# Performance work log

Hardware: AMD Instinct MI355X
Metric: run time of the kernel (lower is better)

The kernel has to match this reference:

```python
import jax, jax.numpy as jnp
import numpy as np

N, P, D = 128, 256, 256
H, M = 16, 32            # num_heads, head_dim; output_dim = H*M = 512
OUT, HID = H * M, 2048


def setup_inputs() -> dict:
    key = jax.random.key(0)
    ks = jax.random.split(key, 7)
    s = 0.02
    return {
        "x": jax.random.normal(ks[0], (N, P, D), jnp.float32),
        "qkv_temporal": jax.random.normal(ks[1], (3, D, H, M), jnp.float32) * s,
        "qkv_point": jax.random.normal(ks[2], (3, H, M, H, M), jnp.float32) * s,
        "W1": jax.random.normal(ks[3], (OUT, HID), jnp.float32) * s,
        "b1": jnp.zeros((HID,), jnp.float32),
        "W2": jax.random.normal(ks[4], (HID, OUT), jnp.float32) * s,
        "b2": jnp.zeros((OUT,), jnp.float32),
    }


def reference(x, qkv_temporal, qkv_point, W1, b1, W2, b2):
    # ---- temporal attention (over frames i/I, per point j) ----
    qkv = jnp.einsum('wdhm,ijd->whmij', qkv_temporal, x)     # (3,H,M,N,P)
    q, k, v = qkv[0], qkv[1], qkv[2]
    scores = jnp.einsum('hmij,hmIj->hiIj', q, k)             # (H,N,N,P)
    weights = jax.nn.softmax(scores, axis=2)
    # NOTE: label order 'hIij' (positional) matches the original source exactly
    temporal = jnp.einsum('hIij,hmIj->hmij', weights, v)     # (H,M,N,P)
    # ---- point attention (over points j/J, per frame i) ----
    qkv = jnp.einsum('whmHM,HMij->whmij', qkv_point, temporal)  # (3,H,M,N,P)
    q, k, v = qkv[0], qkv[1], qkv[2]
    scores = jnp.einsum('hmij,hmiJ->hijJ', q, k)             # (H,N,P,P)
    weights = jax.nn.softmax(scores, axis=-1)
    pa = jnp.einsum('hijJ,hmiJ->ijhm', weights, v)           # (N,P,H,M)
    pa = pa.reshape(pa.shape[0], pa.shape[1], -1)            # (N,P,H*M)
    # ---- two-layer MLP (no activation, matching the source) ----
    h = pa @ W1 + b1
    return h @ W2 + b2
```

## Files before the change

### kernel.cpp

```cpp
#include <hip/hip_runtime.h>
#include <cstddef>
#include <cstdint>

constexpr int Nf = 128, Pp = 256, Dd = 256, Hh = 16, Mm = 32;
constexpr int OUTC = 512, HID = 2048, C3 = 1536;

typedef short short8 __attribute__((ext_vector_type(8)));
typedef float f32x4 __attribute__((ext_vector_type(4)));

__device__ inline unsigned short f2bf(float f) {
  unsigned u = __float_as_uint(f);
  u += 0x7fffu + ((u >> 16) & 1u);
  return (unsigned short)(u >> 16);
}
__device__ inline unsigned pk2(float a, float b) {
  return (unsigned)f2bf(a) | ((unsigned)f2bf(b) << 16);
}

__global__ __launch_bounds__(256) void conv_x(const float* __restrict__ x,
                                              short* __restrict__ xb) {
  int idx = blockIdx.x * 256 + threadIdx.x;
  const float4* s = (const float4*)x + (size_t)idx * 2;
  float4 a = s[0], c = s[1];
  uint4 o;
  o.x = pk2(a.x, a.y); o.y = pk2(a.z, a.w);
  o.z = pk2(c.x, c.y); o.w = pk2(c.z, c.w);
  ((uint4*)xb)[idx] = o;
}

__global__ __launch_bounds__(256) void transpose_to_bf16(const float* __restrict__ in,
                                                         short* __restrict__ out,
                                                         int R, int C) {
  __shared__ float tile[64 * 65];
  const int t = threadIdx.x;
  const int rb = blockIdx.y * 64, cb = blockIdx.x * 64;
  const size_t sl = (size_t)blockIdx.z * R * C;
#pragma unroll
  for (int u = 0; u < 4; ++u) {
    int r = (t >> 4) + u * 16, c4 = (t & 15) * 4;
    float4 v = *(const float4*)(in + sl + (size_t)(rb + r) * C + cb + c4);
    tile[r * 65 + c4 + 0] = v.x;
    tile[r * 65 + c4 + 1] = v.y;
    tile[r * 65 + c4 + 2] = v.z;
    tile[r * 65 + c4 + 3] = v.w;
  }
  __syncthreads();
#pragma unroll
  for (int u = 0; u < 2; ++u) {
    int id = t + u * 256;
    int n = id >> 3, kg = id & 7;
    float a[8];
#pragma unroll
    for (int q = 0; q < 8; ++q) a[q] = tile[(kg * 8 + q) * 65 + n];
    uint4 o;
    o.x = pk2(a[0], a[1]); o.y = pk2(a[2], a[3]);
    o.z = pk2(a[4], a[5]); o.w = pk2(a[6], a[7]);
    *(uint4*)(out + sl + (size_t)(cb + n) * R + rb + kg * 8) = o;
  }
}

__global__ void repack_b2t(const float* __restrict__ Wp, short* __restrict__ B2t) {
  int idx = blockIdx.x * 256 + threadIdx.x;
  int c = idx >> 9, k = idx & 511;
  int w = c >> 9, h = (c >> 5) & 15, m = c & 31;
  int HH = k >> 5, MM = k & 31;
  B2t[idx] = (short)f2bf(Wp[(((w * Hh + h) * Mm + m) * Hh + HH) * Mm + MM]);
}

__global__ __launch_bounds__(256) void wc_splitk(const short* __restrict__ A,
                                                 const short* __restrict__ Bt,
                                                 float* __restrict__ part) {
  __shared__ short As[128 * 32];
  __shared__ short Bs[128 * 32];
  const int t = threadIdx.x;
  const int wv = t >> 6, ln = t & 63;
  const int wr = wv >> 1, wc = wv & 1;
  const int lr = ln & 15, kq = ln >> 4;
  const int row0 = blockIdx.y * 128, col0 = blockIdx.x * 128;
  const int k0 = blockIdx.z * 256;

  f32x4 acc[4][4];
#pragma unroll
  for (int i = 0; i < 4; ++i)
#pragma unroll
    for (int j = 0; j < 4; ++j) acc[i][j] = {0.f, 0.f, 0.f, 0.f};

  for (int kt = k0; kt < k0 + 256; kt += 32) {
#pragma unroll
    for (int u = 0; u < 2; ++u) {
      int seg = wv * 128 + u * 64 + ln;
      int r = seg >> 2, kg = seg & 3;
      const short* gp = A + (size_t)(row0 + r) * HID + kt + kg * 8;
      __builtin_amdgcn_global_load_lds(
          (const __attribute__((address_space(1))) void*)gp,
          (__attribute__((address_space(3))) void*)&As[(wv * 128 + u * 64) * 8], 16, 0, 0);
    }
#pragma unroll
    for (int u = 0; u < 2; ++u) {
      int seg = wv * 128 + u * 64 + ln;
      int r = seg >> 2, kg = seg & 3;
      const short* gp = Bt + (size_t)(col0 + r) * HID + kt + kg * 8;
      __builtin_amdgcn_global_load_lds(
          (const __attribute__((address_space(1))) void*)gp,
          (__attribute__((address_space(3))) void*)&Bs[(wv * 128 + u * 64) * 8], 16, 0, 0);
    }
    __syncthreads();
    short8 a[4], b[4];
#pragma unroll
    for (int ti = 0; ti < 4; ++ti)
      a[ti] = *(const short8*)&As[(wr * 64 + ti * 16 + lr) * 32 + kq * 8];
#pragma unroll
    for (int tj = 0; tj < 4; ++tj)
      b[tj] = *(const short8*)&Bs[(wc * 64 + tj * 16 + lr) * 32 + kq * 8];
#pragma unroll
    for (int ti = 0; ti < 4; ++ti)
#pragma unroll
      for (int tj = 0; tj < 4; ++tj)
        acc[ti][tj] = __builtin_amdgcn_mfma_f32_16x16x32_bf16(a[ti], b[tj], acc[ti][tj], 0, 0, 0);
    __syncthreads();
  }

#pragma unroll
  for (int tj = 0; tj < 4; ++tj) {
    int gcol = col0 + wc * 64 + tj * 16 + lr;
#pragma unroll
    for (int ti = 0; ti < 4; ++ti)
#pragma unroll
      for (int rg = 0; rg < 4; ++rg) {
        int grow = row0 + wr * 64 + ti * 16 + kq * 4 + rg;
        part[((size_t)blockIdx.z * 512 + grow) * 512 + gcol] = acc[ti][tj][rg];
      }
  }
}

__global__ __launch_bounds__(256) void wc_reduce(const float* __restrict__ part,
                                                 short* __restrict__ Wct) {
  int idx = blockIdx.x * 256 + threadIdx.x;
  float s = 0.f;
#pragma unroll
  for (int z = 0; z < 8; ++z) s += part[(size_t)z * 262144 + idx];
  Wct[idx] = (short)f2bf(s);
}

__global__ __launch_bounds__(256) void bc_partial(const float* __restrict__ b1,
                                                  const float* __restrict__ W2,
                                                  float* __restrict__ part) {
  const int z = blockIdx.x;
  const int t = threadIdx.x;
  float s0 = 0.f, s1 = 0.f;
#pragma unroll
  for (int hh = 0; hh < 32; ++hh) {
    int h = z * 32 + hh;
    float bv = b1[h];
    s0 += bv * W2[(size_t)h * OUTC + t];
    s1 += bv * W2[(size_t)h * OUTC + t + 256];
  }
  part[z * OUTC + t] = s0;
  part[z * OUTC + t + 256] = s1;
}

__global__ __launch_bounds__(256) void bc_finish(const float* __restrict__ part,
                                                 const float* __restrict__ b2,
                                                 float* __restrict__ bc) {
  int o = blockIdx.x * 256 + threadIdx.x;
  float s = b2[o];
#pragma unroll
  for (int z = 0; z < 64; ++z) s += part[z * OUTC + o];
  bc[o] = s;
}

template <int KDIM, int NCOLS, int AMAP, int EPI, int OUTT>
__global__ __launch_bounds__(256) void gemm_mfma(const short* __restrict__ A,
                                                 const short* __restrict__ Bt,
                                                 void* __restrict__ Cv,
                                                 const float* __restrict__ bias,
                                                 int j0, int pshift, int pc) {
  __shared__ short As[2][128 * 32];
  __shared__ short Bs[2][128 * 32];
  const int t = threadIdx.x;
  const int wv = t >> 6, ln = t & 63;
  const int wr = wv >> 1, wc = wv & 1;
  const int lr = ln & 15, kq = ln >> 4;

  constexpr int NBX = NCOLS / 128;
  constexpr int NT = KDIM / 32;
  int lin = blockIdx.y * NBX + blockIdx.x;
  int nblk = gridDim.x * gridDim.y;
  int bx, by;
  if ((nblk & 7) == 0) {
    int per = nblk >> 3;
    int id = (lin & 7) * per + (lin >> 3);
    bx = id % NBX; by = id / NBX;
  } else {
    bx = blockIdx.x; by = blockIdx.y;
  }
  const int row0 = by * 128, col0 = bx * 128;

  const int seg0 = wv * 128 + ln;
  const int seg1 = wv * 128 + 64 + ln;
  const int r0 = seg0 >> 2, kg0 = seg0 & 3;
  const int r1 = seg1 >> 2, kg1 = seg1 & 3;
  size_t arow0, arow1;
  {
    int rr = row0 + r0;
    if (AMAP == 0) arow0 = (size_t)rr;
    else { int i = rr >> pshift, jj = rr & (pc - 1); arow0 = (size_t)((i << 8) + j0 + jj); }
    rr = row0 + r1;
    if (AMAP == 0) arow1 = (size_t)rr;
    else { int i = rr >> pshift, jj = rr & (pc - 1); arow1 = (size_t)((i << 8) + j0 + jj); }
  }
  const size_t brow0 = (size_t)(col0 + r0), brow1 = (size_t)(col0 + r1);

  auto stage = [&](int buf, int tk) {
    const int kt = tk * 32;
    __builtin_amdgcn_global_load_lds(
        (const __attribute__((address_space(1))) void*)(A + arow0 * KDIM + kt + kg0 * 8),
        (__attribute__((address_space(3))) void*)&As[buf][(wv * 128) * 8], 16, 0, 0);
    __builtin_amdgcn_global_load_lds(
        (const __attribute__((address_space(1))) void*)(A + arow1 * KDIM + kt + kg1 * 8),
        (__attribute__((address_space(3))) void*)&As[buf][(wv * 128 + 64) * 8], 16, 0, 0);
    __builtin_amdgcn_global_load_lds(
        (const __attribute__((address_space(1))) void*)(Bt + brow0 * KDIM + kt + kg0 * 8),
        (__attribute__((address_space(3))) void*)&Bs[buf][(wv * 128) * 8], 16, 0, 0);
    __builtin_amdgcn_global_load_lds(
        (const __attribute__((address_space(1))) void*)(Bt + brow1 * KDIM + kt + kg1 * 8),
        (__attribute__((address_space(3))) void*)&Bs[buf][(wv * 128 + 64) * 8], 16, 0, 0);
  };

  f32x4 acc[4][4];
#pragma unroll
  for (int i = 0; i < 4; ++i)
#pragma unroll
    for (int j = 0; j < 4; ++j) acc[i][j] = {0.f, 0.f, 0.f, 0.f};

  stage(0, 0);
  stage(1, 1);
  asm volatile("s_waitcnt vmcnt(4)" ::: "memory");
  __builtin_amdgcn_s_barrier();

  for (int tk = 0; tk < NT; ++tk) {
    const int cur = tk & 1;
    short8 a[4], b[4];
#pragma unroll
    for (int ti = 0; ti < 4; ++ti)
      a[ti] = *(const short8*)&As[cur][(wr * 64 + ti * 16 + lr) * 32 + kq * 8];
#pragma unroll
    for (int tj = 0; tj < 4; ++tj)
      b[tj] = *(const short8*)&Bs[cur][(wc * 64 + tj * 16 + lr) * 32 + kq * 8];
    __builtin_amdgcn_sched_barrier(0);
    asm volatile("s_waitcnt lgkmcnt(0)" ::: "memory");
    __builtin_amdgcn_sched_barrier(0);
    if (tk + 1 < NT) {
      __builtin_amdgcn_s_barrier();
      if (tk + 2 < NT) stage(cur, tk + 2);
    }
#pragma unroll
    for (int ti = 0; ti < 4; ++ti)
#pragma unroll
      for (int tj = 0; tj < 4; ++tj)
        acc[ti][tj] = __builtin_amdgcn_mfma_f32_16x16x32_bf16(a[ti], b[tj], acc[ti][tj], 0, 0, 0);
    if (tk + 1 < NT) {
      if (tk + 2 < NT) {
        asm volatile("s_waitcnt vmcnt(4)" ::: "memory");
      } else {
        asm volatile("s_waitcnt vmcnt(0)" ::: "memory");
      }
      __builtin_amdgcn_s_barrier();
      __builtin_amdgcn_sched_barrier(0);
    }
  }

#pragma unroll
  for (int tj = 0; tj < 4; ++tj) {
    int gcol = col0 + wc * 64 + tj * 16 + lr;
    float bv = (EPI == 0) ? bias[gcol] : 0.f;
#pragma unroll
    for (int ti = 0; ti < 4; ++ti) {
#pragma unroll
      for (int rg = 0; rg < 4; ++rg) {
        int grow = row0 + wr * 64 + ti * 16 + kq * 4 + rg;
        float val = acc[ti][tj][rg];
        if (EPI == 0) {
          val += bv;
          if (OUTT == 0) ((short*)Cv)[(size_t)grow * NCOLS + gcol] = (short)f2bf(val);
          else           ((float*)Cv)[(size_t)grow * NCOLS + gcol] = val;
        } else {
          int w = gcol >> 9, h = (gcol >> 5) & 15, m = gcol & 31;
          size_t addr;
          if (EPI == 1) {
            int i = grow >> pshift, jj = grow & (pc - 1);
            addr = (((size_t)(w * Hh + h) * pc + jj) * Nf + i) * Mm + m;
          } else {
            int ii = grow >> 8, j = grow & 255;
            addr = (((size_t)(w * Hh + h) * pc + ii) * Pp + j) * Mm + m;
          }
          ((short*)Cv)[addr] = (short)f2bf(val);
        }
      }
    }
  }
}

__global__ __launch_bounds__(256) void temporal_attn_mfma(const short* __restrict__ T,
                                                          short* __restrict__ At,
                                                          int j0, int jcShift) {
  constexpr int QsO = 0, KsO = 4096, VtO = 8192, WtO = 12544, RsO = 29952;
  __shared__ __align__(16) short lds[30464];
  float* rs = (float*)&lds[RsO];
  const int JC = 1 << jcShift;
  const int h  = blockIdx.x >> jcShift;
  const int jj = blockIdx.x & (JC - 1);
  const int t  = threadIdx.x;
  const int wv = t >> 6, ln = t & 63;
  const int wr = wv >> 1, wc = wv & 1;
  const int lr = ln & 15, kq = ln >> 4;
  const size_t WC = (size_t)(Hh << jcShift) * 4096;
  const short* qb = T + (size_t)(h * JC + jj) * 4096;
  const short* kb = qb + WC;
  const short* vb = qb + 2 * WC;

#pragma unroll
  for (int u = 0; u < 2; ++u) {
    int seg = wv * 2 + u;
    __builtin_amdgcn_global_load_lds(
        (const __attribute__((address_space(1))) void*)(qb + seg * 512 + ln * 8),
        (__attribute__((address_space(3))) void*)&lds[QsO + seg * 512], 16, 0, 0);
    __builtin_amdgcn_global_load_lds(
        (const __attribute__((address_space(1))) void*)(kb + seg * 512 + ln * 8),
        (__attribute__((address_space(3))) void*)&lds[KsO + seg * 512], 16, 0, 0);
  }
#pragma unroll
  for (int u = 0; u < 2; ++u) {
    int idx = t + u * 256;
    int I = idx >> 2, m0 = (idx & 3) * 8;
    uint4 v = *(const uint4*)(vb + idx * 8);
    const short* vs = (const short*)&v;
#pragma unroll
    for (int q = 0; q < 8; ++q) lds[VtO + (m0 + q) * 136 + I] = vs[q];
  }
  __syncthreads();

  short8 af[4], bf[4];
#pragma unroll
  for (int ti = 0; ti < 4; ++ti)
    af[ti] = *(const short8*)&lds[QsO + (wr * 64 + ti * 16 + lr) * 32 + kq * 8];
#pragma unroll
  for (int tj = 0; tj < 4; ++tj)
    bf[tj] = *(const short8*)&lds[KsO + (wc * 64 + tj * 16 + lr) * 32 + kq * 8];
  f32x4 e[4][4];
#pragma unroll
  for (int ti = 0; ti < 4; ++ti)
#pragma unroll
    for (int tj = 0; tj < 4; ++tj) e[ti][tj] = {0.f, 0.f, 0.f, 0.f};
#pragma unroll
  for (int ti = 0; ti < 4; ++ti)
#pragma unroll
    for (int tj = 0; tj < 4; ++tj)
      e[ti][tj] = __builtin_amdgcn_mfma_f32_16x16x32_bf16(af[ti], bf[tj], e[ti][tj], 0, 0, 0);

  float part[4][4];
#pragma unroll
  for (int ti = 0; ti < 4; ++ti)
#pragma unroll
    for (int r = 0; r < 4; ++r) {
      float p = 0.f;
#pragma unroll
      for (int tj = 0; tj < 4; ++tj) {
        float ex = __expf(e[ti][tj][r]);
        e[ti][tj][r] = ex;
        p += ex;
      }
      part[ti][r] = p;
    }
#pragma unroll
  for (int msk = 1; msk <= 8; msk <<= 1)
#pragma unroll
    for (int ti = 0; ti < 4; ++ti)
#pragma unroll
      for (int r = 0; r < 4; ++r)
        part[ti][r] += __shfl_xor(part[ti][r], msk, 64);
  if (lr == 0) {
#pragma unroll
    for (int ti = 0; ti < 4; ++ti)
#pragma unroll
      for (int r = 0; r < 4; ++r)
        rs[wc * 128 + wr * 64 + ti * 16 + kq * 4 + r] = part[ti][r];
  }
  __syncthreads();

#pragma unroll
  for (int ti = 0; ti < 4; ++ti) {
#pragma unroll
    for (int r = 0; r < 4; ++r) {
      int I = wr * 64 + ti * 16 + kq * 4 + r;
      float inv = 1.f / (rs[I] + rs[128 + I]);
#pragma unroll
      for (int tj = 0; tj < 4; ++tj) e[ti][tj][r] *= inv;
    }
#pragma unroll
    for (int tj = 0; tj < 4; ++tj) {
      int i = wc * 64 + tj * 16 + lr;
      int Ib = wr * 64 + ti * 16 + kq * 4;
      uint2 pk;
      pk.x = pk2(e[ti][tj][0], e[ti][tj][1]);
      pk.y = pk2(e[ti][tj][2], e[ti][tj][3]);
      *(uint2*)&lds[WtO + i * 136 + Ib] = pk;
    }
  }
  __syncthreads();

  f32x4 o[2][2];
#pragma unroll
  for (int tr = 0; tr < 2; ++tr)
#pragma unroll
    for (int tm = 0; tm < 2; ++tm) o[tr][tm] = {0.f, 0.f, 0.f, 0.f};
#pragma unroll
  for (int ks = 0; ks < 4; ++ks) {
    short8 ea[2], vf[2];
#pragma unroll
    for (int tr = 0; tr < 2; ++tr)
      ea[tr] = *(const short8*)&lds[WtO + (wv * 32 + tr * 16 + lr) * 136 + ks * 32 + kq * 8];
#pragma unroll
    for (int tm = 0; tm < 2; ++tm)
      vf[tm] = *(const short8*)&lds[VtO + (tm * 16 + lr) * 136 + ks * 32 + kq * 8];
#pragma unroll
    for (int tr = 0; tr < 2; ++tr)
#pragma unroll
      for (int tm = 0; tm < 2; ++tm)
        o[tr][tm] = __builtin_amdgcn_mfma_f32_16x16x32_bf16(ea[tr], vf[tm], o[tr][tm], 0, 0, 0);
  }
#pragma unroll
  for (int tr = 0; tr < 2; ++tr)
#pragma unroll
    for (int tm = 0; tm < 2; ++tm)
#pragma unroll
      for (int r = 0; r < 4; ++r) {
        int row = wv * 32 + tr * 16 + kq * 4 + r;
        lds[row * 40 + tm * 16 + lr] = (short)f2bf(o[tr][tm][r]);
      }
  __syncthreads();
#pragma unroll
  for (int u = 0; u < 2; ++u) {
    int idx = t + u * 256;
    int i = idx >> 2, mg = idx & 3;
    uint4 vv = *(const uint4*)&lds[i * 40 + mg * 8];
    *(uint4*)(At + ((size_t)(i * Pp + j0 + jj) * OUTC + h * 32 + mg * 8)) = vv;
  }
}

__global__ __launch_bounds__(256) void point_attn_mfma(const short* __restrict__ P,
                                                       short* __restrict__ PA,
                                                       int icShift) {
  constexpr int QsO = 0, KsO = 4096, VtO = 8192, EO = 12544, CsO = 29952;
  __shared__ __align__(16) short lds[30720];
  float* cs    = (float*)&lds[CsO];
  float* denom = cs + 256;
  const int IC = 1 << icShift;
  const int bx = blockIdx.x;
  const int h    = bx >> (icShift + 1);
  const int rem  = bx & ((IC << 1) - 1);
  const int ii   = rem >> 1;
  const int half = rem & 1;
  const int t  = threadIdx.x;
  const int wv = t >> 6, ln = t & 63;
  const int wr = wv >> 1, wc = wv & 1;
  const int lr = ln & 15, kq = ln >> 4;
  const size_t WC = (size_t)(Hh << icShift) * 8192;
  const short* qb = P + (size_t)(h * IC + ii) * 8192 + half * 4096;
  const short* kb = P + WC + (size_t)(h * IC + ii) * 8192;
  const short* vb = kb + WC;

  f32x4 o[2][2];
#pragma unroll
  for (int tr = 0; tr < 2; ++tr)
#pragma unroll
    for (int tm = 0; tm < 2; ++tm) o[tr][tm] = {0.f, 0.f, 0.f, 0.f};

  for (int chunk = 0; chunk < 2; ++chunk) {
    const int Jb = chunk * 128;
    if (chunk) __syncthreads();
#pragma unroll
    for (int u = 0; u < 2; ++u) {
      int seg = wv * 2 + u;
      __builtin_amdgcn_global_load_lds(
          (const __attribute__((address_space(1))) void*)(kb + Jb * 32 + seg * 512 + ln * 8),
          (__attribute__((address_space(3))) void*)&lds[KsO + seg * 512], 16, 0, 0);
    }
    if (chunk == 0) {
#pragma unroll
      for (int u = 0; u < 2; ++u) {
        int seg = wv * 2 + u;
        __builtin_amdgcn_global_load_lds(
            (const __attribute__((address_space(1))) void*)(qb + seg * 512 + ln * 8),
            (__attribute__((address_space(3))) void*)&lds[QsO + seg * 512], 16, 0, 0);
      }
      if (t < 128) denom[t] = 0.f;
    }
#pragma unroll
    for (int u = 0; u < 2; ++u) {
      int idx = t + u * 256;
      int Jl = idx >> 2, m0 = (idx & 3) * 8;
      uint4 v = *(const uint4*)(vb + Jb * 32 + idx * 8);
      const short* vs = (const short*)&v;
#pragma unroll
      for (int q = 0; q < 8; ++q) lds[VtO + (m0 + q) * 136 + Jl] = vs[q];
    }
    __syncthreads();

    short8 af[4], bf[4];
#pragma unroll
    for (int ti = 0; ti < 4; ++ti)
      af[ti] = *(const short8*)&lds[KsO + (wr * 64 + ti * 16 + lr) * 32 + kq * 8];
#pragma unroll
    for (int tj = 0; tj < 4; ++tj)
      bf[tj] = *(const short8*)&lds[QsO + (wc * 64 + tj * 16 + lr) * 32 + kq * 8];
    f32x4 e[4][4];
#pragma unroll
    for (int ti = 0; ti < 4; ++ti)
#pragma unroll
      for (int tj = 0; tj < 4; ++tj) e[ti][tj] = {0.f, 0.f, 0.f, 0.f};
#pragma unroll
    for (int ti = 0; ti < 4; ++ti)
#pragma unroll
      for (int tj = 0; tj < 4; ++tj)
        e[ti][tj] = __builtin_amdgcn_mfma_f32_16x16x32_bf16(af[ti], bf[tj], e[ti][tj], 0, 0, 0);

    float cp[4] = {0.f, 0.f, 0.f, 0.f};
#pragma unroll
    for (int ti = 0; ti < 4; ++ti)
#pragma unroll
      for (int tj = 0; tj < 4; ++tj)
#pragma unroll
        for (int r = 0; r < 4; ++r) {
          float ex = __expf(e[ti][tj][r]);
          e[ti][tj][r] = ex;
          cp[tj] += ex;
        }
#pragma unroll
    for (int tj = 0; tj < 4; ++tj) {
      cp[tj] += __shfl_xor(cp[tj], 16, 64);
      cp[tj] += __shfl_xor(cp[tj], 32, 64);
    }
    if (kq == 0) {
#pragma unroll
      for (int tj = 0; tj < 4; ++tj)
        cs[wr * 128 + wc * 64 + tj * 16 + lr] = cp[tj];
    }
#pragma unroll
    for (int ti = 0; ti < 4; ++ti)
#pragma unroll
      for (int tj = 0; tj < 4; ++tj) {
        int j  = wc * 64 + tj * 16 + lr;
        int Jl = wr * 64 + ti * 16 + kq * 4;
        uint2 pk;
        pk.x = pk2(e[ti][tj][0], e[ti][tj][1]);
        pk.y = pk2(e[ti][tj][2], e[ti][tj][3]);
        *(uint2*)&lds[EO + j * 136 + Jl] = pk;
      }
    __syncthreads();
    if (t < 128) denom[t] += cs[t] + cs[128 + t];

#pragma unroll
    for (int ks = 0; ks < 4; ++ks) {
      short8 ea[2], vf[2];
#pragma unroll
      for (int tr = 0; tr < 2; ++tr)
        ea[tr] = *(const short8*)&lds[EO + (wv * 32 + tr * 16 + lr) * 136 + ks * 32 + kq * 8];
#pragma unroll
      for (int tm = 0; tm < 2; ++tm)
        vf[tm] = *(const short8*)&lds[VtO + (tm * 16 + lr) * 136 + ks * 32 + kq * 8];
#pragma unroll
      for (int tr = 0; tr < 2; ++tr)
#pragma unroll
        for (int tm = 0; tm < 2; ++tm)
          o[tr][tm] = __builtin_amdgcn_mfma_f32_16x16x32_bf16(ea[tr], vf[tm], o[tr][tm], 0, 0, 0);
    }
  }
  __syncthreads();

#pragma unroll
  for (int tr = 0; tr < 2; ++tr)
#pragma unroll
    for (int r = 0; r < 4; ++r) {
      int row = wv * 32 + tr * 16 + kq * 4 + r;
      float rinv = 1.f / denom[row];
#pragma unroll
      for (int tm = 0; tm < 2; ++tm)
        lds[row * 40 + tm * 16 + lr] = (short)f2bf(o[tr][tm][r] * rinv);
    }
  __syncthreads();
#pragma unroll
  for (int u = 0; u < 2; ++u) {
    int idx = t + u * 256;
    int jl = idx >> 2, mg = idx & 3;
    uint4 vv = *(const uint4*)&lds[jl * 40 + mg * 8];
    *(uint4*)(PA + ((size_t)(ii * Pp + half * 128 + jl) * OUTC + h * 32 + mg * 8)) = vv;
  }
}

extern "C" void kernel_launch(void* const* d_in, const int* in_sizes, int n_in,
                              void* d_out, int out_size, void* d_ws, size_t ws_size,
                              hipStream_t stream) {
  const float* x  = (const float*)d_in[0];
  const float* Wt = (const float*)d_in[1];
  const float* Wp = (const float*)d_in[2];
  const float* W1 = (const float*)d_in[3];
  const float* b1 = (const float*)d_in[4];
  const float* W2 = (const float*)d_in[5];
  const float* b2 = (const float*)d_in[6];
  float* out = (float*)d_out;
  short* ws  = (short*)d_ws;

  const size_t fixedH = 8388608 + 16777216 + 393216 + 786432 + 1048576 + 1048576
                      + 262144 + 1024 + 4194304 + 65536;
  size_t availH = ws_size / 2;
  size_t chF; int JC, IC;
  if      (availH >= fixedH + 50331648) { chF = 50331648; JC = 256; IC = 128; }
  else if (availH >= fixedH + 12582912) { chF = 12582912; JC = 64;  IC = 32;  }
  else if (availH >= fixedH + 6291456)  { chF = 6291456;  JC = 32;  IC = 16;  }
  else                                  { chF = 3145728;  JC = 16;  IC = 8;   }
  short* CH  = ws;
  short* xbf = CH + chF;
  short* At  = xbf + 8388608;
  short* B1t = At + 16777216;
  short* B2t = B1t + 393216;
  short* W1b = B2t + 786432;
  short* W2t = W1b + 1048576;
  short* Wct = W2t + 1048576;
  float* bcF   = (float*)(Wct + 262144);
  float* partF = (float*)(Wct + 262144 + 1024);
  float* bcP   = (float*)(Wct + 262144 + 1024 + 4194304);
  const int jcS = __builtin_ctz((unsigned)JC);
  const int icS = __builtin_ctz((unsigned)IC);

  conv_x<<<4096, 256, 0, stream>>>(x, xbf);
  conv_x<<<512, 256, 0, stream>>>(W1, W1b);
  transpose_to_bf16<<<dim3(8, 4, 3), 256, 0, stream>>>(Wt, B1t, 256, 512);
  repack_b2t<<<3072, 256, 0, stream>>>(Wp, B2t);
  transpose_to_bf16<<<dim3(8, 32, 1), 256, 0, stream>>>(W2, W2t, 2048, 512);

  wc_splitk<<<dim3(4, 4, 8), 256, 0, stream>>>(W2t, W1b, partF);
  wc_reduce<<<1024, 256, 0, stream>>>(partF, Wct);
  bc_partial<<<64, 256, 0, stream>>>(b1, W2, bcP);
  bc_finish<<<2, 256, 0, stream>>>(bcP, b2, bcF);

  if (JC == 256) {
    gemm_mfma<256, 1536, 0, 1, 0><<<dim3(12, 256), 256, 0, stream>>>(xbf, B1t, CH, nullptr, 0, 8, 256);
    temporal_attn_mfma<<<Hh * 256, 256, 0, stream>>>(CH, At, 0, 8);
    gemm_mfma<512, 1536, 0, 2, 0><<<dim3(12, 256), 256, 0, stream>>>(At, B2t, CH, nullptr, 0, 0, 128);
    point_attn_mfma<<<Hh * 128 * 2, 256, 0, stream>>>(CH, At, 7);
  } else {
    for (int j0 = 0; j0 < Pp; j0 += JC) {
      gemm_mfma<256, 1536, 1, 1, 0><<<dim3(12, JC), 256, 0, stream>>>(xbf, B1t, CH, nullptr, j0, jcS, JC);
      temporal_attn_mfma<<<Hh * JC, 256, 0, stream>>>(CH, At, j0, jcS);
    }
    for (int i0 = 0; i0 < Nf; i0 += IC) {
      short* Arows = At + (size_t)i0 * Pp * OUTC;
      gemm_mfma<512, 1536, 0, 2, 0><<<dim3(12, IC * 2), 256, 0, stream>>>(Arows, B2t, CH, nullptr, 0, 0, IC);
      point_attn_mfma<<<Hh * IC * 2, 256, 0, stream>>>(CH, Arows, icS);
    }
  }

  gemm_mfma<512, 512, 0, 0, 1><<<dim3(4, 256), 256, 0, stream>>>(At, Wct, out, bcF, 0, 0, 0);
}
```

Baseline: 408.5 us.

## Swizzle GEMM LDS tiles and stage scattered epilogue through LDS for vector stores

The GEMM LDS tiles now use an XOR swizzle on the k-group slot to reduce bank conflicts when reading MFMA operands. For the head-scattered outputs (EPI 2 and a new EPI 3), the accumulator is first written into shared memory and then stored to global memory as contiguous 16-byte vectors, replacing scattered 2-byte stores. A new AMAP 3 row mapping orders the first projection GEMM so each 128-row tile covers all frames of one point, which makes its output tile contiguous in the per-head temporal layout. These changes cost an extra barrier and an LDS round trip in the epilogue, and make the index arithmetic more complex.

```diff
diff --git a/kernel.cpp b/kernel.cpp
--- a/kernel.cpp
+++ b/kernel.cpp
@@ -175,8 +175,7 @@
                                                  void* __restrict__ Cv,
                                                  const float* __restrict__ bias,
                                                  int j0, int pshift, int pc) {
-  __shared__ short As[2][128 * 32];
-  __shared__ short Bs[2][128 * 32];
+  __shared__ __align__(16) short SH[16384];
   const int t = threadIdx.x;
   const int wv = t >> 6, ln = t & 63;
   const int wr = wv >> 1, wc = wv & 1;
@@ -198,15 +197,18 @@
 
   const int seg0 = wv * 128 + ln;
   const int seg1 = wv * 128 + 64 + ln;
-  const int r0 = seg0 >> 2, kg0 = seg0 & 3;
-  const int r1 = seg1 >> 2, kg1 = seg1 & 3;
+  const int r0 = seg0 >> 2, r1 = seg1 >> 2;
+  const int kg0 = (seg0 & 3) ^ ((r0 >> 1) & 3);
+  const int kg1 = (seg1 & 3) ^ ((r1 >> 1) & 3);
   size_t arow0, arow1;
   {
     int rr = row0 + r0;
-    if (AMAP == 0) arow0 = (size_t)rr;
+    if (AMAP == 0)      arow0 = (size_t)rr;
+    else if (AMAP == 3) arow0 = (size_t)(((rr & 127) << 8) + (rr >> 7));
     else { int i = rr >> pshift, jj = rr & (pc - 1); arow0 = (size_t)((i << 8) + j0 + jj); }
     rr = row0 + r1;
-    if (AMAP == 0) arow1 = (size_t)rr;
+    if (AMAP == 0)      arow1 = (size_t)rr;
+    else if (AMAP == 3) arow1 = (size_t)(((rr & 127) << 8) + (rr >> 7));
     else { int i = rr >> pshift, jj = rr & (pc - 1); arow1 = (size_t)((i << 8) + j0 + jj); }
   }
   const size_t brow0 = (size_t)(col0 + r0), brow1 = (size_t)(col0 + r1);
@@ -215,16 +217,16 @@
     const int kt = tk * 32;
     __builtin_amdgcn_global_load_lds(
         (const __attribute__((address_space(1))) void*)(A + arow0 * KDIM + kt + kg0 * 8),
-        (__attribute__((address_space(3))) void*)&As[buf][(wv * 128) * 8], 16, 0, 0);
+        (__attribute__((address_space(3))) void*)&SH[buf * 4096 + (wv * 128) * 8], 16, 0, 0);
     __builtin_amdgcn_global_load_lds(
         (const __attribute__((address_space(1))) void*)(A + arow1 * KDIM + kt + kg1 * 8),
-        (__attribute__((address_space(3))) void*)&As[buf][(wv * 128 + 64) * 8], 16, 0, 0);
+        (__attribute__((address_space(3))) void*)&SH[buf * 4096 + (wv * 128 + 64) * 8], 16, 0, 0);
     __builtin_amdgcn_global_load_lds(
         (const __attribute__((address_space(1))) void*)(Bt + brow0 * KDIM + kt + kg0 * 8),
-        (__attribute__((address_space(3))) void*)&Bs[buf][(wv * 128) * 8], 16, 0, 0);
+        (__attribute__((address_space(3))) void*)&SH[8192 + buf * 4096 + (wv * 128) * 8], 16, 0, 0);
     __builtin_amdgcn_global_load_lds(
         (const __attribute__((address_space(1))) void*)(Bt + brow1 * KDIM + kt + kg1 * 8),
-        (__attribute__((address_space(3))) void*)&Bs[buf][(wv * 128 + 64) * 8], 16, 0, 0);
+        (__attribute__((address_space(3))) void*)&SH[8192 + buf * 4096 + (wv * 128 + 64) * 8], 16, 0, 0);
   };
 
   f32x4 acc[4][4];
@@ -232,6 +234,8 @@
   for (int i = 0; i < 4; ++i)
 #pragma unroll
     for (int j = 0; j < 4; ++j) acc[i][j] = {0.f, 0.f, 0.f, 0.f};
+
+  const int slot = kq ^ ((lr >> 1) & 3);
 
   stage(0, 0);
   stage(1, 1);
@@ -243,10 +247,10 @@
     short8 a[4], b[4];
 #pragma unroll
     for (int ti = 0; ti < 4; ++ti)
-      a[ti] = *(const short8*)&As[cur][(wr * 64 + ti * 16 + lr) * 32 + kq * 8];
+      a[ti] = *(const short8*)&SH[cur * 4096 + (wr * 64 + ti * 16 + lr) * 32 + slot * 8];
 #pragma unroll
     for (int tj = 0; tj < 4; ++tj)
-      b[tj] = *(const short8*)&Bs[cur][(wc * 64 + tj * 16 + lr) * 32 + kq * 8];
+      b[tj] = *(const short8*)&SH[8192 + cur * 4096 + (wc * 64 + tj * 16 + lr) * 32 + slot * 8];
     __builtin_amdgcn_sched_barrier(0);
     asm volatile("s_waitcnt lgkmcnt(0)" ::: "memory");
     __builtin_amdgcn_sched_barrier(0);
@@ -270,33 +274,56 @@
     }
   }
 
-#pragma unroll
-  for (int tj = 0; tj < 4; ++tj) {
-    int gcol = col0 + wc * 64 + tj * 16 + lr;
-    float bv = (EPI == 0) ? bias[gcol] : 0.f;
-#pragma unroll
-    for (int ti = 0; ti < 4; ++ti) {
-#pragma unroll
-      for (int rg = 0; rg < 4; ++rg) {
-        int grow = row0 + wr * 64 + ti * 16 + kq * 4 + rg;
-        float val = acc[ti][tj][rg];
-        if (EPI == 0) {
-          val += bv;
-          if (OUTT == 0) ((short*)Cv)[(size_t)grow * NCOLS + gcol] = (short)f2bf(val);
-          else           ((float*)Cv)[(size_t)grow * NCOLS + gcol] = val;
-        } else {
-          int w = gcol >> 9, h = (gcol >> 5) & 15, m = gcol & 31;
-          size_t addr;
-          if (EPI == 1) {
+  if (EPI == 0 || EPI == 1) {
+#pragma unroll
+    for (int tj = 0; tj < 4; ++tj) {
+      int gcol = col0 + wc * 64 + tj * 16 + lr;
+      float bv = (EPI == 0) ? bias[gcol] : 0.f;
+#pragma unroll
+      for (int ti = 0; ti < 4; ++ti) {
+#pragma unroll
+        for (int rg = 0; rg < 4; ++rg) {
+          int grow = row0 + wr * 64 + ti * 16 + kq * 4 + rg;
+          float val = acc[ti][tj][rg];
+          if (EPI == 0) {
+            val += bv;
+            if (OUTT == 0) ((short*)Cv)[(size_t)grow * NCOLS + gcol] = (short)f2bf(val);
+            else           ((float*)Cv)[(size_t)grow * NCOLS + gcol] = val;
+          } else {
+            int w = gcol >> 9, h = (gcol >> 5) & 15, m = gcol & 31;
             int i = grow >> pshift, jj = grow & (pc - 1);
-            addr = (((size_t)(w * Hh + h) * pc + jj) * Nf + i) * Mm + m;
-          } else {
-            int ii = grow >> 8, j = grow & 255;
-            addr = (((size_t)(w * Hh + h) * pc + ii) * Pp + j) * Mm + m;
+            size_t addr = (((size_t)(w * Hh + h) * pc + jj) * Nf + i) * Mm + m;
+            ((short*)Cv)[addr] = (short)f2bf(val);
           }
-          ((short*)Cv)[addr] = (short)f2bf(val);
         }
       }
+    }
+  } else {
+    __builtin_amdgcn_s_barrier();
+#pragma unroll
+    for (int ti = 0; ti < 4; ++ti)
+#pragma unroll
+      for (int tj = 0; tj < 4; ++tj) {
+        int c = wc * 64 + tj * 16 + lr;
+        int q = c >> 5, m = c & 31;
+#pragma unroll
+        for (int rg = 0; rg < 4; ++rg) {
+          int g = wr * 64 + ti * 16 + kq * 4 + rg;
+          SH[q * 4096 + g * 32 + (m ^ ((g & 4) << 2))] = (short)f2bf(acc[ti][tj][rg]);
+        }
+      }
+    __syncthreads();
+#pragma unroll
+    for (int u = 0; u < 8; ++u) {
+      int id = u * 256 + t;
+      int q = id >> 9, rem = id & 511, g = rem >> 2, mc = (rem & 3) * 8;
+      uint4 v = *(const uint4*)&SH[q * 4096 + g * 32 + (mc ^ ((g & 4) << 2))];
+      int gc = col0 + q * 32;
+      int w = gc >> 9, h = (gc >> 5) & 15;
+      size_t base;
+      if (EPI == 3) base = ((size_t)(w * Hh + h) * 256 + (row0 >> 7)) * 4096;
+      else          base = (((size_t)(w * Hh + h) * pc + (row0 >> 8)) * 256 + (row0 & 255)) * 32;
+      *(uint4*)((short*)Cv + base + g * 32 + mc) = v;
     }
   }
 }
@@ -645,7 +672,7 @@
   bc_finish<<<2, 256, 0, stream>>>(bcP, b2, bcF);
 
   if (JC == 256) {
-    gemm_mfma<256, 1536, 0, 1, 0><<<dim3(12, 256), 256, 0, stream>>>(xbf, B1t, CH, nullptr, 0, 8, 256);
+    gemm_mfma<256, 1536, 3, 3, 0><<<dim3(12, 256), 256, 0, stream>>>(xbf, B1t, CH, nullptr, 0, 0, 256);
     temporal_attn_mfma<<<Hh * 256, 256, 0, stream>>>(CH, At, 0, 8);
     gemm_mfma<512, 1536, 0, 2, 0><<<dim3(12, 256), 256, 0, stream>>>(At, B2t, CH, nullptr, 0, 0, 128);
     point_attn_mfma<<<Hh * 128 * 2, 256, 0, stream>>>(CH, At, 7);
```

After: 368.2 us. 9.9% less time.
